# Performance work log

Measured on AMD Instinct MI355X. Metric: run time of the kernel, lower is better.

The kernel has to match this reference:

```python
import jax, jax.numpy as jnp
import numpy as np

N = 100000          # num_nodes
E = 1_600_000       # num_edges
F = 16              # node_features
HID = 32            # DCRNN hidden size (hardcoded in DCRNNModel)
OUT = 12            # output_len
K = 2               # diffusion steps (intended DCRNN; see notes)
CIN = F + HID       # DConv input channels: concat([X, H])


def setup_inputs() -> dict:
    key = jax.random.key(0)
    ks = jax.random.split(key, 12)
    x = jax.random.normal(ks[0], (N, F), dtype=jnp.float32)
    edge_index = jax.random.randint(ks[1], (2, E), 0, N, dtype=jnp.int32)
    edge_weight = jax.random.uniform(ks[2], (E,), jnp.float32, minval=0.05, maxval=1.0)
    sc = 0.1
    W_z = jax.random.normal(ks[3], (2, K, CIN, HID), jnp.float32) * sc
    b_z = jax.random.normal(ks[4], (HID,), jnp.float32) * sc
    W_r = jax.random.normal(ks[5], (2, K, CIN, HID), jnp.float32) * sc
    b_r = jax.random.normal(ks[6], (HID,), jnp.float32) * sc
    W_h = jax.random.normal(ks[7], (2, K, CIN, HID), jnp.float32) * sc
    b_h = jax.random.normal(ks[8], (HID,), jnp.float32) * sc
    lin_W = jax.random.normal(ks[9], (HID, OUT), jnp.float32) * sc
    lin_b = jax.random.normal(ks[10], (OUT,), jnp.float32) * sc
    return {"x": x, "edge_index": edge_index, "edge_weight": edge_weight,
            "W_z": W_z, "b_z": b_z, "W_r": W_r, "b_r": b_r,
            "W_h": W_h, "b_h": b_h, "lin_W": lin_W, "lin_b": lin_b}


def reference(x, edge_index, edge_weight, W_z, b_z, W_r, b_r, W_h, b_h, lin_W, lin_b):
    src, dst = edge_index[0], edge_index[1]
    # weighted out/in degrees (as in to_dense_adj row/col sums)
    deg_out = jax.ops.segment_sum(edge_weight, src, num_segments=N)
    deg_in = jax.ops.segment_sum(edge_weight, dst, num_segments=N)
    inv_out_e = (1.0 / deg_out)[src][:, None]  # [E,1] per-edge 1/deg_out(src)
    inv_in_e = (1.0 / deg_in)[dst][:, None]    # [E,1] per-edge 1/deg_in(dst)

    def dconv(Xc, W, b):
        # K=0 term (both diffusion directions share Tx_0 = X)
        H = Xc @ W[0, 0] + Xc @ W[1, 0]
        # forward diffusion: out[dst] += (1/deg_out[src]) * Xc[src]
        T_o = jax.ops.segment_sum(inv_out_e * Xc[src], dst, num_segments=N)
        # reverse diffusion: out[src] += (1/deg_in[dst]) * Xc[dst]
        T_i = jax.ops.segment_sum(inv_in_e * Xc[dst], src, num_segments=N)
        return H + T_o @ W[0, 1] + T_i @ W[1, 1] + b

    H0 = jnp.zeros((N, HID), dtype=x.dtype)
    XH = jnp.concatenate([x, H0], axis=1)           # [N, F+HID]
    Z = jax.nn.sigmoid(dconv(XH, W_z, b_z))         # update gate
    R = jax.nn.sigmoid(dconv(XH, W_r, b_r))         # reset gate
    XHr = jnp.concatenate([x, H0 * R], axis=1)
    H_tilde = jnp.tanh(dconv(XHr, W_h, b_h))
    H = Z * H0 + (1.0 - Z) * H_tilde                # [N, HID]
    return jax.nn.relu(H) @ lin_W + lin_b           # [N, OUT]
```

## Files before the change

### kernel.cpp

```cpp
#include <hip/hip_runtime.h>
#include <math.h>

#define N_NODES 100000
#define N_EDGES 1600000
#define NF 16
#define HID 32
#define OUTD 12
#define CIN3 48

#define NB   1024
#define RNG  98
#define PBLK 256
#define CHUNK ((N_EDGES + PBLK - 1) / PBLK)
#define CAP   2560
#define CAPT  10

typedef unsigned int uint;


__global__ __launch_bounds__(256)
void p1_count(const int* __restrict__ ei, uint* __restrict__ cntD, uint* __restrict__ cntS) {
    __shared__ uint cD[NB], cS[NB];
    int t = threadIdx.x, blk = blockIdx.x;
    for (int i = t; i < NB; i += 256) { cD[i] = 0; cS[i] = 0; }
    __syncthreads();
    int lo = blk * CHUNK, hi = min(lo + CHUNK, N_EDGES);
    for (int e = lo + t; e < hi; e += 256) {
        uint s = (uint)ei[e];
        uint d = (uint)ei[N_EDGES + e];
        atomicAdd(&cS[s / RNG], 1u);
        atomicAdd(&cD[d / RNG], 1u);
    }
    __syncthreads();
    for (int i = t; i < NB; i += 256) {
        cntD[i * PBLK + blk] = cD[i];
        cntS[i * PBLK + blk] = cS[i];
    }
}

__global__ __launch_bounds__(256)
void p2a_rowsum(const uint* __restrict__ cntD, const uint* __restrict__ cntS,
                uint* __restrict__ totD, uint* __restrict__ totS) {
    __shared__ uint red[256];
    int t = threadIdx.x;
    bool isS = blockIdx.x >= NB;
    int b = isS ? (blockIdx.x - NB) : blockIdx.x;
    const uint* cnt = isS ? cntS : cntD;
    red[t] = cnt[b * PBLK + t];
    __syncthreads();
    for (int s = 128; s > 0; s >>= 1) { if (t < s) red[t] += red[t + s]; __syncthreads(); }
    if (t == 0) (isS ? totS : totD)[b] = red[0];
}

__global__ __launch_bounds__(256)
void p2b_scan(const uint* __restrict__ totD, const uint* __restrict__ totS,
              uint* __restrict__ baseD, uint* __restrict__ baseS) {
    __shared__ uint part[256];
    int t = threadIdx.x;
    for (int dir = 0; dir < 2; ++dir) {
        const uint* tot = dir ? totS : totD;
        uint* base = dir ? baseS : baseD;
        uint v[4]; uint s = 0;
#pragma unroll
        for (int k = 0; k < 4; ++k) { v[k] = tot[t * 4 + k]; s += v[k]; }
        part[t] = s;
        __syncthreads();
        if (t == 0) {
            uint a = 0;
            for (int k = 0; k < 256; ++k) { uint x = part[k]; part[k] = a; a += x; }
            base[NB] = a;
        }
        __syncthreads();
        uint a = part[t];
#pragma unroll
        for (int k = 0; k < 4; ++k) { base[t * 4 + k] = a; a += v[k]; }
        __syncthreads();
    }
}

__global__ __launch_bounds__(256)
void p2c_rowscan(const uint* __restrict__ cntD, const uint* __restrict__ cntS,
                 const uint* __restrict__ baseD, const uint* __restrict__ baseS,
                 uint* __restrict__ offD, uint* __restrict__ offS) {
    __shared__ uint row[PBLK];
    int t = threadIdx.x;
    bool isS = blockIdx.x >= NB;
    int b = isS ? (blockIdx.x - NB) : blockIdx.x;
    const uint* cnt = isS ? cntS : cntD;
    const uint* base = isS ? baseS : baseD;
    uint* off = isS ? offS : offD;
    row[t] = cnt[b * PBLK + t];
    __syncthreads();
    if (t == 0) {
        uint a = base[b];
        for (int k = 0; k < PBLK; ++k) { uint v = row[k]; row[k] = a; a += v; }
    }
    __syncthreads();
    off[b * PBLK + t] = row[t];
}

__global__ __launch_bounds__(256)
void p3_scatter(const int* __restrict__ ei, const float* __restrict__ ew,
                const uint* __restrict__ offD, const uint* __restrict__ offS,
                uint2* __restrict__ recD, uint2* __restrict__ recS) {
    __shared__ uint curD[NB], curS[NB];
    int t = threadIdx.x, blk = blockIdx.x;
    for (int b = t; b < NB; b += 256) {
        curD[b] = offD[b * PBLK + blk];
        curS[b] = offS[b * PBLK + blk];
    }
    __syncthreads();
    int lo = blk * CHUNK, hi = min(lo + CHUNK, N_EDGES);
    for (int e = lo + t; e < hi; e += 256) {
        uint s = (uint)ei[e];
        uint d = (uint)ei[N_EDGES + e];
        uint w = __float_as_uint(ew[e]);
        uint bd = d / RNG, dl = d - bd * RNG;
        uint p = atomicAdd(&curD[bd], 1u);
        recD[p] = make_uint2(s | (dl << 20), w);
        uint bs = s / RNG, sl = s - bs * RNG;
        uint p2 = atomicAdd(&curS[bs], 1u);
        recS[p2] = make_uint2(d | (sl << 20), w);
    }
}

__global__ __launch_bounds__(256)
void kdeg(const uint2* __restrict__ recD, const uint2* __restrict__ recS,
          const uint* __restrict__ baseD, const uint* __restrict__ baseS,
          float* __restrict__ inv_in, float* __restrict__ inv_out) {
    __shared__ float dacc[RNG];
    int t = threadIdx.x;
    bool isS = blockIdx.x >= NB;
    int b = isS ? (blockIdx.x - NB) : blockIdx.x;
    const uint2* rec = isS ? recS : recD;
    const uint* base = isS ? baseS : baseD;
    float* inv = isS ? inv_out : inv_in;
    for (int i = t; i < RNG; i += 256) dacc[i] = 0.0f;
    __syncthreads();
    uint lo = base[b], hi = base[b + 1];
    for (uint e = lo + t; e < hi; e += 256) {
        uint2 r = rec[e];
        atomicAdd(&dacc[r.x >> 20], __uint_as_float(r.y));
    }
    __syncthreads();
    int n0 = b * RNG;
    for (int i = t; i < RNG; i += 256) {
        int n = n0 + i;
        if (n < N_NODES) inv[n] = 1.0f / dacc[i];
    }
}

__global__ __launch_bounds__(256)
void p4_sorted(const uint2* __restrict__ recD, const uint2* __restrict__ recS,
               const uint* __restrict__ baseD, const uint* __restrict__ baseS,
               const float* __restrict__ x,
               const float* __restrict__ inv_out, const float* __restrict__ inv_in,
               float* __restrict__ To, float* __restrict__ Ti) {
    __shared__ uint sorted[CAP];
    __shared__ uint scnt[RNG];
    __shared__ uint cstart[RNG + 1];
    __shared__ uint scur[RNG];
    int t = threadIdx.x;
    bool isS = blockIdx.x >= NB;
    int b = isS ? (blockIdx.x - NB) : blockIdx.x;
    const uint2* rec = isS ? recS : recD;
    const uint* base = isS ? baseS : baseD;
    const float* inv = isS ? inv_in : inv_out;
    float* out = isS ? Ti : To;

    int f = t & 15, s = t >> 4;
    uint lo = base[b], hi = base[b + 1];

    float acc[7];
#pragma unroll
    for (int k = 0; k < 7; ++k) acc[k] = 0.0f;

    for (uint chunk = lo; chunk < hi; chunk += CAP) {
        uint n_in = min(hi - chunk, (uint)CAP);
        for (int i = t; i < RNG; i += 256) scnt[i] = 0;
        __syncthreads();
        uint stash[CAPT];
#pragma unroll
        for (int k = 0; k < CAPT; ++k) {
            uint i = (uint)(k * 256 + t);
            if (i < n_in) {
                uint r = rec[chunk + i].x;
                stash[k] = r;
                atomicAdd(&scnt[r >> 20], 1u);
            }
        }
        __syncthreads();
        if (t == 0) {
            uint a = 0;
            for (int n = 0; n < RNG; ++n) { cstart[n] = a; a += scnt[n]; }
            cstart[RNG] = a;
        }
        __syncthreads();
        for (int i = t; i < RNG; i += 256) scur[i] = cstart[i];
        __syncthreads();
#pragma unroll
        for (int k = 0; k < CAPT; ++k) {
            uint i = (uint)(k * 256 + t);
            if (i < n_in) {
                uint r = stash[k];
                uint p = atomicAdd(&scur[r >> 20], 1u);
                sorted[p] = r;
            }
        }
        __syncthreads();
#pragma unroll
        for (int k = 0; k < 7; ++k) {
            int n = s + 16 * k;
            if (n < RNG) {
                uint j = cstart[n], j1 = cstart[n + 1];
                for (; j + 8 <= j1; j += 8) {
                    uint p0 = sorted[j],     p1 = sorted[j + 1], p2 = sorted[j + 2], p3 = sorted[j + 3];
                    uint p4 = sorted[j + 4], p5 = sorted[j + 5], p6 = sorted[j + 6], p7 = sorted[j + 7];
                    uint o0 = p0 & 0xFFFFFu, o1 = p1 & 0xFFFFFu, o2 = p2 & 0xFFFFFu, o3 = p3 & 0xFFFFFu;
                    uint o4 = p4 & 0xFFFFFu, o5 = p5 & 0xFFFFFu, o6 = p6 & 0xFFFFFu, o7 = p7 & 0xFFFFFu;
                    float g0 = x[(size_t)o0 * NF + f], g1 = x[(size_t)o1 * NF + f];
                    float g2 = x[(size_t)o2 * NF + f], g3 = x[(size_t)o3 * NF + f];
                    float g4 = x[(size_t)o4 * NF + f], g5 = x[(size_t)o5 * NF + f];
                    float g6 = x[(size_t)o6 * NF + f], g7 = x[(size_t)o7 * NF + f];
                    float w0 = inv[o0], w1 = inv[o1], w2 = inv[o2], w3 = inv[o3];
                    float w4 = inv[o4], w5 = inv[o5], w6 = inv[o6], w7 = inv[o7];
                    acc[k] += g0 * w0 + g1 * w1 + g2 * w2 + g3 * w3
                            + g4 * w4 + g5 * w5 + g6 * w6 + g7 * w7;
                }
                for (; j < j1; ++j) {
                    uint p = sorted[j];
                    uint o = p & 0xFFFFFu;
                    acc[k] += x[(size_t)o * NF + f] * inv[o];
                }
            }
        }
        __syncthreads();
    }

#pragma unroll
    for (int k = 0; k < 7; ++k) {
        int n = s + 16 * k;
        if (n < RNG) {
            size_t g = (size_t)b * RNG + n;
            if (g < N_NODES) out[g * NF + f] = acc[k];
        }
    }
}

__global__ void wprep_kernel(const float* __restrict__ Wz, const float* __restrict__ Wh,
                             float* __restrict__ WzT, float* __restrict__ WhT) {
    int t = blockIdx.x * blockDim.x + threadIdx.x;
    if (t >= 2 * CIN3 * HID) return;
    const float* W = (t < CIN3 * HID) ? Wz : Wh;
    float* WT      = (t < CIN3 * HID) ? WzT : WhT;
    int i = (t < CIN3 * HID) ? t : (t - CIN3 * HID);
    int c = i / HID;
    int h = i - c * HID;
    float v;
    if (c < 16)      v = W[(0 * 48 + c) * 32 + h] + W[(2 * 48 + c) * 32 + h];
    else if (c < 32) v = W[(1 * 48 + (c - 16)) * 32 + h];
    else             v = W[(3 * 48 + (c - 32)) * 32 + h];
    WT[h * CIN3 + c] = v;
}

__global__ __launch_bounds__(256)
void node_kernel(const float* __restrict__ x, const float* __restrict__ To,
                 const float* __restrict__ Ti,
                 const float* __restrict__ WzT, const float* __restrict__ WhT,
                 const float* __restrict__ bz, const float* __restrict__ bh,
                 const float* __restrict__ linW, const float* __restrict__ linb,
                 float* __restrict__ out) {
    __shared__ __align__(16) float sWz[HID * CIN3];
    __shared__ __align__(16) float sWh[HID * CIN3];
    __shared__ __align__(16) float sBz[HID], sBh[HID];
    __shared__ __align__(16) float sLW[HID * OUTD];
    __shared__ __align__(16) float sLb[OUTD];

    for (int i = threadIdx.x; i < HID * CIN3; i += 256) { sWz[i] = WzT[i]; sWh[i] = WhT[i]; }
    if (threadIdx.x < HID) { sBz[threadIdx.x] = bz[threadIdx.x]; sBh[threadIdx.x] = bh[threadIdx.x]; }
    for (int i = threadIdx.x; i < HID * OUTD; i += 256) sLW[i] = linW[i];
    if (threadIdx.x < OUTD) sLb[threadIdx.x] = linb[threadIdx.x];
    __syncthreads();

    int n = blockIdx.x * 256 + threadIdx.x;
    if (n >= N_NODES) return;

    float feat[CIN3];
#pragma unroll
    for (int q = 0; q < 4; ++q) {
        float4 v = ((const float4*)(x + (size_t)n * NF))[q];
        feat[q*4+0]=v.x; feat[q*4+1]=v.y; feat[q*4+2]=v.z; feat[q*4+3]=v.w;
    }
#pragma unroll
    for (int q = 0; q < 4; ++q) {
        float4 v = ((const float4*)(To + (size_t)n * NF))[q];
        feat[16+q*4+0]=v.x; feat[16+q*4+1]=v.y; feat[16+q*4+2]=v.z; feat[16+q*4+3]=v.w;
    }
#pragma unroll
    for (int q = 0; q < 4; ++q) {
        float4 v = ((const float4*)(Ti + (size_t)n * NF))[q];
        feat[32+q*4+0]=v.x; feat[32+q*4+1]=v.y; feat[32+q*4+2]=v.z; feat[32+q*4+3]=v.w;
    }

    float o[OUTD];
#pragma unroll
    for (int j = 0; j < OUTD; ++j) o[j] = sLb[j];

#pragma unroll 2
    for (int h = 0; h < HID; ++h) {
        float az = sBz[h];
        float ah = sBh[h];
        const float4* wz4 = (const float4*)(sWz + h * CIN3);
        const float4* wh4 = (const float4*)(sWh + h * CIN3);
#pragma unroll
        for (int q = 0; q < CIN3 / 4; ++q) {
            float4 wz = wz4[q];
            float4 wh = wh4[q];
            float f0 = feat[q*4+0], f1 = feat[q*4+1], f2 = feat[q*4+2], f3 = feat[q*4+3];
            az += f0*wz.x + f1*wz.y + f2*wz.z + f3*wz.w;
            ah += f0*wh.x + f1*wh.y + f2*wh.z + f3*wh.w;
        }
        float z  = 1.0f / (1.0f + expf(-az));
        float ht = tanhf(ah);
        float r  = fmaxf((1.0f - z) * ht, 0.0f);
#pragma unroll
        for (int j = 0; j < OUTD; ++j) o[j] += r * sLW[h * OUTD + j];
    }

    float4* op = (float4*)(out + (size_t)n * OUTD);
    op[0] = make_float4(o[0], o[1], o[2],  o[3]);
    op[1] = make_float4(o[4], o[5], o[6],  o[7]);
    op[2] = make_float4(o[8], o[9], o[10], o[11]);
}

__global__ void zero_kernel(float* __restrict__ p, int n) {
    int i = blockIdx.x * blockDim.x + threadIdx.x;
    int stride = gridDim.x * blockDim.x;
    for (; i < n; i += stride) p[i] = 0.0f;
}
__global__ void degree_compact(const int* __restrict__ ei, const float* __restrict__ ew,
                               float* __restrict__ deg_out, float* __restrict__ deg_in) {
    int e = blockIdx.x * blockDim.x + threadIdx.x;
    if (e >= N_EDGES) return;
    atomicAdd(&deg_out[ei[e]], ew[e]);
    atomicAdd(&deg_in[ei[N_EDGES + e]], ew[e]);
}
__global__ void rcp_compact(float* __restrict__ a, float* __restrict__ b) {
    int n = blockIdx.x * blockDim.x + threadIdx.x;
    if (n >= N_NODES) return;
    a[n] = 1.0f / a[n]; b[n] = 1.0f / b[n];
}
__global__ __launch_bounds__(256)
void scatter_kernel(const int* __restrict__ ei, const float* __restrict__ x,
                    const float* __restrict__ inv_out, const float* __restrict__ inv_in,
                    float* __restrict__ To, float* __restrict__ Ti) {
    int t = blockIdx.x * blockDim.x + threadIdx.x;
    if (t >= N_EDGES * NF) return;
    int e = t >> 4, f = t & 15;
    int src = ei[e], dst = ei[N_EDGES + e];
    atomicAdd(&To[dst * NF + f], x[src * NF + f] * inv_out[src]);
    atomicAdd(&Ti[src * NF + f], x[dst * NF + f] * inv_in[dst]);
}

extern "C" void kernel_launch(void* const* d_in, const int* in_sizes, int n_in,
                              void* d_out, int out_size, void* d_ws, size_t ws_size,
                              hipStream_t stream) {
    const float* x    = (const float*)d_in[0];
    const int*   ei   = (const int*)  d_in[1];
    const float* ew   = (const float*)d_in[2];
    const float* Wz   = (const float*)d_in[3];
    const float* bz   = (const float*)d_in[4];
    const float* Wh   = (const float*)d_in[7];
    const float* bh   = (const float*)d_in[8];
    const float* linW = (const float*)d_in[9];
    const float* linb = (const float*)d_in[10];

    float* ws = (float*)d_ws;

    size_t off = 0;
    uint2* recD = (uint2*)(ws + off); off += 2 * (size_t)N_EDGES;
    uint2* recS = (uint2*)(ws + off); off += 2 * (size_t)N_EDGES;
    uint* cntD  = (uint*)(ws + off);  off += (size_t)NB * PBLK;
    uint* cntS  = (uint*)(ws + off);  off += (size_t)NB * PBLK;
    uint* offD  = (uint*)(ws + off);  off += (size_t)NB * PBLK;
    uint* offS  = (uint*)(ws + off);  off += (size_t)NB * PBLK;
    uint* totD  = (uint*)(ws + off);  off += NB;
    uint* totS  = (uint*)(ws + off);  off += NB;
    uint* baseD = (uint*)(ws + off);  off += NB + 1;
    uint* baseS = (uint*)(ws + off);  off += NB + 1;
    float* inv_out = ws + off;        off += N_NODES;
    float* inv_in  = ws + off;        off += N_NODES;
    float* To   = ws + off;           off += (size_t)NF * N_NODES;
    float* Ti   = ws + off;           off += (size_t)NF * N_NODES;
    float* WzT  = ws + off;           off += CIN3 * HID;
    float* WhT  = ws + off;           off += CIN3 * HID;
    size_t need = off * sizeof(float);

    if (ws_size >= need) {
        p1_count    <<<PBLK,  256, 0, stream>>>(ei, cntD, cntS);
        p2a_rowsum  <<<2*NB,  256, 0, stream>>>(cntD, cntS, totD, totS);
        p2b_scan    <<<1,     256, 0, stream>>>(totD, totS, baseD, baseS);
        p2c_rowscan <<<2*NB,  256, 0, stream>>>(cntD, cntS, baseD, baseS, offD, offS);
        p3_scatter  <<<PBLK,  256, 0, stream>>>(ei, ew, offD, offS, recD, recS);
        kdeg        <<<2*NB,  256, 0, stream>>>(recD, recS, baseD, baseS, inv_in, inv_out);
        wprep_kernel<<<12,    256, 0, stream>>>(Wz, Wh, WzT, WhT);
        p4_sorted   <<<2*NB,  256, 0, stream>>>(recD, recS, baseD, baseS, x, inv_out, inv_in, To, Ti);
        node_kernel <<<(N_NODES + 255) / 256, 256, 0, stream>>>(x, To, Ti, WzT, WhT, bz, bh,
                                                                linW, linb, (float*)d_out);
    } else {
        float* fTo  = ws;
        float* fTi  = ws + 16 * N_NODES;
        float* fIo  = ws + 32 * N_NODES;
        float* fIi  = ws + 33 * N_NODES;
        float* fWzT = ws + 34 * N_NODES;
        float* fWhT = fWzT + CIN3 * HID;
        zero_kernel<<<2048, 256, 0, stream>>>(fTo, 34 * N_NODES);
        degree_compact<<<(N_EDGES + 255) / 256, 256, 0, stream>>>(ei, ew, fIo, fIi);
        rcp_compact<<<(N_NODES + 255) / 256, 256, 0, stream>>>(fIo, fIi);
        scatter_kernel<<<(N_EDGES * NF + 255) / 256, 256, 0, stream>>>(ei, x, fIo, fIi, fTo, fTi);
        wprep_kernel<<<12, 256, 0, stream>>>(Wz, Wh, fWzT, fWhT);
        node_kernel<<<(N_NODES + 255) / 256, 256, 0, stream>>>(x, fTo, fTi, fWzT, fWhT, bz, bh,
                                                               linW, linb, (float*)d_out);
    }
}
```

Baseline: 173.4 us.

## Halve bucket count, double nodes per bucket, and parallelize local bucket scan

```diff
diff --git a/kernel.cpp b/kernel.cpp
--- a/kernel.cpp
+++ b/kernel.cpp
@@ -8,12 +8,13 @@
 #define OUTD 12
 #define CIN3 48
 
-#define NB   1024
-#define RNG  98
-#define PBLK 256
+#define NB   512
+#define RNG  196
+#define PBLK 512
 #define CHUNK ((N_EDGES + PBLK - 1) / PBLK)
-#define CAP   2560
-#define CAPT  10
+#define CAP   3328
+#define CAPT  13
+#define ACCN  13
 
 typedef unsigned int uint;
 
@@ -46,7 +47,7 @@
     bool isS = blockIdx.x >= NB;
     int b = isS ? (blockIdx.x - NB) : blockIdx.x;
     const uint* cnt = isS ? cntS : cntD;
-    red[t] = cnt[b * PBLK + t];
+    red[t] = cnt[b * PBLK + t] + cnt[b * PBLK + 256 + t];
     __syncthreads();
     for (int s = 128; s > 0; s >>= 1) { if (t < s) red[t] += red[t + s]; __syncthreads(); }
     if (t == 0) (isS ? totS : totD)[b] = red[0];
@@ -60,10 +61,8 @@
     for (int dir = 0; dir < 2; ++dir) {
         const uint* tot = dir ? totS : totD;
         uint* base = dir ? baseS : baseD;
-        uint v[4]; uint s = 0;
-#pragma unroll
-        for (int k = 0; k < 4; ++k) { v[k] = tot[t * 4 + k]; s += v[k]; }
-        part[t] = s;
+        uint v0 = tot[t * 2], v1 = tot[t * 2 + 1];
+        part[t] = v0 + v1;
         __syncthreads();
         if (t == 0) {
             uint a = 0;
@@ -72,8 +71,8 @@
         }
         __syncthreads();
         uint a = part[t];
-#pragma unroll
-        for (int k = 0; k < 4; ++k) { base[t * 4 + k] = a; a += v[k]; }
+        base[t * 2] = a;
+        base[t * 2 + 1] = a + v0;
         __syncthreads();
     }
 }
@@ -90,6 +89,7 @@
     const uint* base = isS ? baseS : baseD;
     uint* off = isS ? offS : offD;
     row[t] = cnt[b * PBLK + t];
+    row[256 + t] = cnt[b * PBLK + 256 + t];
     __syncthreads();
     if (t == 0) {
         uint a = base[b];
@@ -97,6 +97,7 @@
     }
     __syncthreads();
     off[b * PBLK + t] = row[t];
+    off[b * PBLK + 256 + t] = row[256 + t];
 }
 
 __global__ __launch_bounds__(256)
@@ -160,6 +161,7 @@
     __shared__ uint scnt[RNG];
     __shared__ uint cstart[RNG + 1];
     __shared__ uint scur[RNG];
+    __shared__ uint sscan[256];
     int t = threadIdx.x;
     bool isS = blockIdx.x >= NB;
     int b = isS ? (blockIdx.x - NB) : blockIdx.x;
@@ -171,9 +173,9 @@
     int f = t & 15, s = t >> 4;
     uint lo = base[b], hi = base[b + 1];
 
-    float acc[7];
-#pragma unroll
-    for (int k = 0; k < 7; ++k) acc[k] = 0.0f;
+    float acc[ACCN];
+#pragma unroll
+    for (int k = 0; k < ACCN; ++k) acc[k] = 0.0f;
 
     for (uint chunk = lo; chunk < hi; chunk += CAP) {
         uint n_in = min(hi - chunk, (uint)CAP);
@@ -190,13 +192,18 @@
             }
         }
         __syncthreads();
-        if (t == 0) {
-            uint a = 0;
-            for (int n = 0; n < RNG; ++n) { cstart[n] = a; a += scnt[n]; }
-            cstart[RNG] = a;
-        }
-        __syncthreads();
-        for (int i = t; i < RNG; i += 256) scur[i] = cstart[i];
+        uint v = (t < RNG) ? scnt[t] : 0u;
+        sscan[t] = v;
+        __syncthreads();
+#pragma unroll
+        for (int d = 1; d < 256; d <<= 1) {
+            uint a = (t >= d) ? sscan[t - d] : 0u;
+            __syncthreads();
+            sscan[t] += a;
+            __syncthreads();
+        }
+        if (t < RNG) { cstart[t] = sscan[t] - v; scur[t] = sscan[t] - v; }
+        if (t == 0) cstart[RNG] = sscan[RNG - 1];
         __syncthreads();
 #pragma unroll
         for (int k = 0; k < CAPT; ++k) {
@@ -209,7 +216,7 @@
         }
         __syncthreads();
 #pragma unroll
-        for (int k = 0; k < 7; ++k) {
+        for (int k = 0; k < ACCN; ++k) {
             int n = s + 16 * k;
             if (n < RNG) {
                 uint j = cstart[n], j1 = cstart[n + 1];
@@ -238,7 +245,7 @@
     }
 
 #pragma unroll
-    for (int k = 0; k < 7; ++k) {
+    for (int k = 0; k < ACCN; ++k) {
         int n = s + 16 * k;
         if (n < RNG) {
             size_t g = (size_t)b * RNG + n;
```

Result: slower. 179.4 us (+3.5%).

## Split edge records into SoA arrays with fixed-point weights and parallel LDS scan

Applied to the files above, without the earlier changes.

```diff
diff --git a/kernel.cpp b/kernel.cpp
--- a/kernel.cpp
+++ b/kernel.cpp
@@ -14,6 +14,7 @@
 #define CHUNK ((N_EDGES + PBLK - 1) / PBLK)
 #define CAP   2560
 #define CAPT  10
+#define ACCN  7
 
 typedef unsigned int uint;
 
@@ -102,7 +103,8 @@
 __global__ __launch_bounds__(256)
 void p3_scatter(const int* __restrict__ ei, const float* __restrict__ ew,
                 const uint* __restrict__ offD, const uint* __restrict__ offS,
-                uint2* __restrict__ recD, uint2* __restrict__ recS) {
+                uint* __restrict__ recXD, uint* __restrict__ recWD,
+                uint* __restrict__ recXS, uint* __restrict__ recWS) {
     __shared__ uint curD[NB], curS[NB];
     int t = threadIdx.x, blk = blockIdx.x;
     for (int b = t; b < NB; b += 256) {
@@ -114,44 +116,47 @@
     for (int e = lo + t; e < hi; e += 256) {
         uint s = (uint)ei[e];
         uint d = (uint)ei[N_EDGES + e];
-        uint w = __float_as_uint(ew[e]);
+        float w = ew[e];
+        uint wfix = (uint)(w * 16777216.0f + 0.5f);
         uint bd = d / RNG, dl = d - bd * RNG;
         uint p = atomicAdd(&curD[bd], 1u);
-        recD[p] = make_uint2(s | (dl << 20), w);
+        recXD[p] = s | (dl << 20);
+        recWD[p] = (dl << 25) | wfix;
         uint bs = s / RNG, sl = s - bs * RNG;
         uint p2 = atomicAdd(&curS[bs], 1u);
-        recS[p2] = make_uint2(d | (sl << 20), w);
-    }
-}
-
-__global__ __launch_bounds__(256)
-void kdeg(const uint2* __restrict__ recD, const uint2* __restrict__ recS,
+        recXS[p2] = d | (sl << 20);
+        recWS[p2] = (sl << 25) | wfix;
+    }
+}
+
+__global__ __launch_bounds__(256)
+void kdeg(const uint* __restrict__ recWD, const uint* __restrict__ recWS,
           const uint* __restrict__ baseD, const uint* __restrict__ baseS,
           float* __restrict__ inv_in, float* __restrict__ inv_out) {
-    __shared__ float dacc[RNG];
+    __shared__ uint dacc[RNG];
     int t = threadIdx.x;
     bool isS = blockIdx.x >= NB;
     int b = isS ? (blockIdx.x - NB) : blockIdx.x;
-    const uint2* rec = isS ? recS : recD;
+    const uint* rec = isS ? recWS : recWD;
     const uint* base = isS ? baseS : baseD;
     float* inv = isS ? inv_out : inv_in;
-    for (int i = t; i < RNG; i += 256) dacc[i] = 0.0f;
+    for (int i = t; i < RNG; i += 256) dacc[i] = 0u;
     __syncthreads();
     uint lo = base[b], hi = base[b + 1];
     for (uint e = lo + t; e < hi; e += 256) {
-        uint2 r = rec[e];
-        atomicAdd(&dacc[r.x >> 20], __uint_as_float(r.y));
+        uint r = rec[e];
+        atomicAdd(&dacc[r >> 25], r & 0x1FFFFFFu);
     }
     __syncthreads();
     int n0 = b * RNG;
     for (int i = t; i < RNG; i += 256) {
         int n = n0 + i;
-        if (n < N_NODES) inv[n] = 1.0f / dacc[i];
-    }
-}
-
-__global__ __launch_bounds__(256)
-void p4_sorted(const uint2* __restrict__ recD, const uint2* __restrict__ recS,
+        if (n < N_NODES) inv[n] = 16777216.0f / (float)dacc[i];
+    }
+}
+
+__global__ __launch_bounds__(256)
+void p4_sorted(const uint* __restrict__ recXD, const uint* __restrict__ recXS,
                const uint* __restrict__ baseD, const uint* __restrict__ baseS,
                const float* __restrict__ x,
                const float* __restrict__ inv_out, const float* __restrict__ inv_in,
@@ -160,10 +165,11 @@
     __shared__ uint scnt[RNG];
     __shared__ uint cstart[RNG + 1];
     __shared__ uint scur[RNG];
+    __shared__ uint sscan[256];
     int t = threadIdx.x;
     bool isS = blockIdx.x >= NB;
     int b = isS ? (blockIdx.x - NB) : blockIdx.x;
-    const uint2* rec = isS ? recS : recD;
+    const uint* rec = isS ? recXS : recXD;
     const uint* base = isS ? baseS : baseD;
     const float* inv = isS ? inv_in : inv_out;
     float* out = isS ? Ti : To;
@@ -171,9 +177,9 @@
     int f = t & 15, s = t >> 4;
     uint lo = base[b], hi = base[b + 1];
 
-    float acc[7];
-#pragma unroll
-    for (int k = 0; k < 7; ++k) acc[k] = 0.0f;
+    float acc[ACCN];
+#pragma unroll
+    for (int k = 0; k < ACCN; ++k) acc[k] = 0.0f;
 
     for (uint chunk = lo; chunk < hi; chunk += CAP) {
         uint n_in = min(hi - chunk, (uint)CAP);
@@ -184,19 +190,24 @@
         for (int k = 0; k < CAPT; ++k) {
             uint i = (uint)(k * 256 + t);
             if (i < n_in) {
-                uint r = rec[chunk + i].x;
+                uint r = rec[chunk + i];
                 stash[k] = r;
                 atomicAdd(&scnt[r >> 20], 1u);
             }
         }
         __syncthreads();
-        if (t == 0) {
-            uint a = 0;
-            for (int n = 0; n < RNG; ++n) { cstart[n] = a; a += scnt[n]; }
-            cstart[RNG] = a;
-        }
-        __syncthreads();
-        for (int i = t; i < RNG; i += 256) scur[i] = cstart[i];
+        uint v = (t < RNG) ? scnt[t] : 0u;
+        sscan[t] = v;
+        __syncthreads();
+#pragma unroll
+        for (int d = 1; d < 256; d <<= 1) {
+            uint a = (t >= d) ? sscan[t - d] : 0u;
+            __syncthreads();
+            sscan[t] += a;
+            __syncthreads();
+        }
+        if (t < RNG) { cstart[t] = sscan[t] - v; scur[t] = sscan[t] - v; }
+        if (t == 0) cstart[RNG] = sscan[RNG - 1];
         __syncthreads();
 #pragma unroll
         for (int k = 0; k < CAPT; ++k) {
@@ -209,7 +220,7 @@
         }
         __syncthreads();
 #pragma unroll
-        for (int k = 0; k < 7; ++k) {
+        for (int k = 0; k < ACCN; ++k) {
             int n = s + 16 * k;
             if (n < RNG) {
                 uint j = cstart[n], j1 = cstart[n + 1];
@@ -238,7 +249,7 @@
     }
 
 #pragma unroll
-    for (int k = 0; k < 7; ++k) {
+    for (int k = 0; k < ACCN; ++k) {
         int n = s + 16 * k;
         if (n < RNG) {
             size_t g = (size_t)b * RNG + n;
@@ -378,8 +389,10 @@
     float* ws = (float*)d_ws;
 
     size_t off = 0;
-    uint2* recD = (uint2*)(ws + off); off += 2 * (size_t)N_EDGES;
-    uint2* recS = (uint2*)(ws + off); off += 2 * (size_t)N_EDGES;
+    uint* recXD = (uint*)(ws + off);  off += (size_t)N_EDGES;
+    uint* recWD = (uint*)(ws + off);  off += (size_t)N_EDGES;
+    uint* recXS = (uint*)(ws + off);  off += (size_t)N_EDGES;
+    uint* recWS = (uint*)(ws + off);  off += (size_t)N_EDGES;
     uint* cntD  = (uint*)(ws + off);  off += (size_t)NB * PBLK;
     uint* cntS  = (uint*)(ws + off);  off += (size_t)NB * PBLK;
     uint* offD  = (uint*)(ws + off);  off += (size_t)NB * PBLK;
@@ -401,10 +414,10 @@
         p2a_rowsum  <<<2*NB,  256, 0, stream>>>(cntD, cntS, totD, totS);
         p2b_scan    <<<1,     256, 0, stream>>>(totD, totS, baseD, baseS);
         p2c_rowscan <<<2*NB,  256, 0, stream>>>(cntD, cntS, baseD, baseS, offD, offS);
-        p3_scatter  <<<PBLK,  256, 0, stream>>>(ei, ew, offD, offS, recD, recS);
-        kdeg        <<<2*NB,  256, 0, stream>>>(recD, recS, baseD, baseS, inv_in, inv_out);
+        p3_scatter  <<<PBLK,  256, 0, stream>>>(ei, ew, offD, offS, recXD, recWD, recXS, recWS);
+        kdeg        <<<2*NB,  256, 0, stream>>>(recWD, recWS, baseD, baseS, inv_in, inv_out);
         wprep_kernel<<<12,    256, 0, stream>>>(Wz, Wh, WzT, WhT);
-        p4_sorted   <<<2*NB,  256, 0, stream>>>(recD, recS, baseD, baseS, x, inv_out, inv_in, To, Ti);
+        p4_sorted   <<<2*NB,  256, 0, stream>>>(recXD, recXS, baseD, baseS, x, inv_out, inv_in, To, Ti);
         node_kernel <<<(N_NODES + 255) / 256, 256, 0, stream>>>(x, To, Ti, WzT, WhT, bz, bh,
                                                                 linW, linb, (float*)d_out);
     } else {
```

After: 211.9 us. +22.2%, slower.
